# Kernel optimization log

Measured on AMD Instinct MI355X. Metric: run time of the kernel, lower is better.

## Reference

```python
import jax, jax.numpy as jnp
import numpy as np

IN_FEATURES = 512
OUT_FEATURES = 128
KERNEL_DIM = 32
BATCH = 128


def setup_inputs() -> dict:
    key = jax.random.key(0)
    kx, kT = jax.random.split(key)
    x = jax.random.normal(kx, (BATCH, IN_FEATURES), dtype=jnp.float32)
    # nn.Parameter initialized with normal(0, 1)
    T = jax.random.normal(kT, (IN_FEATURES, OUT_FEATURES, KERNEL_DIM), dtype=jnp.float32)
    return {"x": x, "T": T}


def reference(x, T):
    B = x.shape[0]
    in_f, out_f, k_dim = T.shape
    # projection: [B, in] @ [in, out*k] -> [B, out, k]
    m = (x @ T.reshape(in_f, out_f * k_dim)).reshape(B, out_f, k_dim)
    # pairwise L1 distance over kernel dim: [B, B, out]
    # original: M = m[None], M_T = m[:, None]; norm = |M - M_T|.sum(3); o_b = exp(-norm).sum(0) - 1
    norm = jnp.abs(m[None, :, :, :] - m[:, None, :, :]).sum(axis=-1)  # [i=B, j=B, out]
    o_b = jnp.exp(-norm).sum(axis=0) - 1.0  # [B, out] (subtract self-distance term exp(0)=1)
    return jnp.concatenate([x, o_b], axis=1)  # [B, in + out]
```

## Files before the change

### kernel.cpp

```cpp
#include <hip/hip_runtime.h>

#define B_SZ    128
#define IN_F    512
#define OUT_F   128
#define NC      4096
#define KD      32
#define OUT_COLS 640
#define MO_PITCH 36
#define AS_PITCH 136
#define BK      128

typedef __attribute__((ext_vector_type(8))) short  bf16x8;
typedef __attribute__((ext_vector_type(4))) float  f32x4;

static __device__ __forceinline__ unsigned short f2bfu(float f) {
    return (unsigned short)(__float_as_uint(f) >> 16);
}

__global__ __launch_bounds__(256) void prep_kernel(
    const float* __restrict__ x, float* __restrict__ out,
    unsigned short* __restrict__ xb)
{
    int idx = blockIdx.x * 256 + threadIdx.x;
    int b = idx >> 7, c4 = idx & 127;
    float4 v = ((const float4*)x)[idx];
    *(float4*)(out + b * OUT_COLS + c4 * 4) = v;
    ushort4 w;
    w.x = f2bfu(v.x); w.y = f2bfu(v.y); w.z = f2bfu(v.z); w.w = f2bfu(v.w);
    *(ushort4*)(xb + idx * 4) = w;
}

__global__ __launch_bounds__(512, 2) void gemm_kernel(
    const unsigned short* __restrict__ xb,
    const float* __restrict__ T,
    float* __restrict__ m)
{
    __shared__ unsigned short as[64 * AS_PITCH];
    __shared__ unsigned short bs[32 * AS_PITCH];

    const int tid  = threadIdx.x;
    const int lane = tid & 63;
    const int w    = tid >> 6;
    const int col  = lane & 15;
    const int q    = lane >> 4;
    const int n0   = blockIdx.x * 32;
    const int m0   = blockIdx.y * 64;
    const int mt   = w >> 1, nt = w & 1;

    f32x4 acc = {0.f, 0.f, 0.f, 0.f};

    for (int k0 = 0; k0 < IN_F; k0 += BK) {
        __syncthreads();
        #pragma unroll
        for (int p = 0; p < 2; ++p) {
            int u = tid + p * 512;
            int row = u >> 4, o8 = u & 15;
            uint4 v = *(const uint4*)(xb + (m0 + row) * IN_F + k0 + o8 * 8);
            *(uint4*)&as[row * AS_PITCH + o8 * 8] = v;
        }
        #pragma unroll
        for (int p = 0; p < 2; ++p) {
            int u = tid + p * 512;
            int kk = u >> 3, nq = u & 7;
            float4 v = *(const float4*)(T + (size_t)(k0 + kk) * NC + n0 + nq * 4);
            int nb = nq * 4;
            bs[(nb + 0) * AS_PITCH + kk] = f2bfu(v.x);
            bs[(nb + 1) * AS_PITCH + kk] = f2bfu(v.y);
            bs[(nb + 2) * AS_PITCH + kk] = f2bfu(v.z);
            bs[(nb + 3) * AS_PITCH + kk] = f2bfu(v.w);
        }
        __syncthreads();
        #pragma unroll
        for (int kt = 0; kt < 4; ++kt) {
            const int krel = kt * 32 + q * 8;
            bf16x8 af = *(const bf16x8*)&as[(mt * 16 + col) * AS_PITCH + krel];
            bf16x8 bf = *(const bf16x8*)&bs[(nt * 16 + col) * AS_PITCH + krel];
            acc = __builtin_amdgcn_mfma_f32_16x16x32_bf16(af, bf, acc, 0, 0, 0);
        }
    }
    float* dst = m + (size_t)(m0 + mt * 16 + q * 4) * NC + n0 + nt * 16 + col;
    dst[0 * NC] = acc[0]; dst[1 * NC] = acc[1];
    dst[2 * NC] = acc[2]; dst[3 * NC] = acc[3];
}

__global__ __launch_bounds__(1024, 4) void pairwise_kernel(
    const float* __restrict__ m,
    float* __restrict__ out)
{
    __shared__ float mo[B_SZ * MO_PITCH];
    __shared__ float psum[64 * 16];

    const int tid   = threadIdx.x;
    const int o     = blockIdx.x >> 1;
    const int jhalf = blockIdx.x & 1;

    {
        const int b = tid >> 3, k4 = tid & 7;
        float4 v = *(const float4*)(m + (size_t)b * NC + o * KD + k4 * 4);
        *(float4*)&mo[b * MO_PITCH + k4 * 4] = v;
    }
    __syncthreads();

    const int jj  = tid & 63;
    const int isl = tid >> 6;
    const int j   = jhalf * 64 + jj;

    float mj[KD];
    #pragma unroll
    for (int k4 = 0; k4 < 8; ++k4) {
        float4 v = *(const float4*)&mo[j * MO_PITCH + k4 * 4];
        mj[k4*4+0] = v.x; mj[k4*4+1] = v.y; mj[k4*4+2] = v.z; mj[k4*4+3] = v.w;
    }

    float s = 0.f;
    const int i0 = isl * 8;
    for (int i = i0; i < i0 + 8; ++i) {
        float norm = 0.f;
        #pragma unroll
        for (int k4 = 0; k4 < 8; ++k4) {
            float4 v = *(const float4*)&mo[i * MO_PITCH + k4 * 4];
            norm += fabsf(mj[k4*4+0] - v.x) + fabsf(mj[k4*4+1] - v.y)
                  + fabsf(mj[k4*4+2] - v.z) + fabsf(mj[k4*4+3] - v.w);
        }
        s += __expf(-norm);
    }
    psum[jj * 16 + isl] = s;
    __syncthreads();
    if (tid < 64) {
        float tot = 0.f;
        #pragma unroll
        for (int u = 0; u < 16; ++u) tot += psum[tid * 16 + u];
        out[(jhalf * 64 + tid) * OUT_COLS + IN_F + o] = tot - 1.0f;
    }
}

extern "C" void kernel_launch(void* const* d_in, const int* in_sizes, int n_in,
                              void* d_out, int out_size, void* d_ws, size_t ws_size,
                              hipStream_t stream) {
    const float* x = (const float*)d_in[0];
    const float* T = (const float*)d_in[1];
    float* out = (float*)d_out;
    float* m = (float*)d_ws;
    unsigned short* xb = (unsigned short*)((char*)d_ws + (2u << 20));

    prep_kernel<<<64, 256, 0, stream>>>(x, out, xb);
    gemm_kernel<<<dim3(128, 2), 512, 0, stream>>>(xb, T, m);
    pairwise_kernel<<<256, 1024, 0, stream>>>(m, out);
}
```

Baseline: 72.87 us.

## Fuse prep, GEMM and pairwise L1 kernels into a single kernel

```diff
diff --git a/kernel.cpp b/kernel.cpp
--- a/kernel.cpp
+++ b/kernel.cpp
@@ -1,13 +1,10 @@
 #include <hip/hip_runtime.h>
 
-#define B_SZ    128
 #define IN_F    512
-#define OUT_F   128
 #define NC      4096
-#define KD      32
 #define OUT_COLS 640
+#define AS_PITCH 136
 #define MO_PITCH 36
-#define AS_PITCH 136
 #define BK      128
 
 typedef __attribute__((ext_vector_type(8))) short  bf16x8;
@@ -16,54 +13,54 @@
 static __device__ __forceinline__ unsigned short f2bfu(float f) {
     return (unsigned short)(__float_as_uint(f) >> 16);
 }
-
-__global__ __launch_bounds__(256) void prep_kernel(
-    const float* __restrict__ x, float* __restrict__ out,
-    unsigned short* __restrict__ xb)
-{
-    int idx = blockIdx.x * 256 + threadIdx.x;
-    int b = idx >> 7, c4 = idx & 127;
-    float4 v = ((const float4*)x)[idx];
-    *(float4*)(out + b * OUT_COLS + c4 * 4) = v;
-    ushort4 w;
-    w.x = f2bfu(v.x); w.y = f2bfu(v.y); w.z = f2bfu(v.z); w.w = f2bfu(v.w);
-    *(ushort4*)(xb + idx * 4) = w;
+static __device__ __forceinline__ unsigned int pack2(float lo, float hi) {
+    return (__float_as_uint(lo) >> 16) | (__float_as_uint(hi) & 0xFFFF0000u);
 }
 
-__global__ __launch_bounds__(512, 2) void gemm_kernel(
-    const unsigned short* __restrict__ xb,
+__global__ __launch_bounds__(1024, 4) void fused_kernel(
+    const float* __restrict__ x,
     const float* __restrict__ T,
-    float* __restrict__ m)
+    float* __restrict__ out)
 {
-    __shared__ unsigned short as[64 * AS_PITCH];
-    __shared__ unsigned short bs[32 * AS_PITCH];
+    __shared__ __align__(16) char smem[51968];
+    unsigned short* as = (unsigned short*)smem;
+    unsigned short* bs = (unsigned short*)(smem + 34816);
+    float* mo   = (float*)smem;
+    float* psum = (float*)(smem + 43520);
 
-    const int tid  = threadIdx.x;
-    const int lane = tid & 63;
-    const int w    = tid >> 6;
-    const int col  = lane & 15;
-    const int q    = lane >> 4;
-    const int n0   = blockIdx.x * 32;
-    const int m0   = blockIdx.y * 64;
-    const int mt   = w >> 1, nt = w & 1;
+    const int tid   = threadIdx.x;
+    const int lane  = tid & 63;
+    const int w     = tid >> 6;
+    const int col   = lane & 15;
+    const int q     = lane >> 4;
+    const int o     = blockIdx.x >> 1;
+    const int jhalf = blockIdx.x & 1;
+    const int mt    = w >> 1;
+    const int nt    = w & 1;
+
+    if (tid < 64) {
+        int idx = blockIdx.x * 64 + tid;
+        int b = idx >> 7, c4 = idx & 127;
+        float4 v = ((const float4*)x)[idx];
+        *(float4*)(out + b * OUT_COLS + c4 * 4) = v;
+    }
 
     f32x4 acc = {0.f, 0.f, 0.f, 0.f};
-
     for (int k0 = 0; k0 < IN_F; k0 += BK) {
         __syncthreads();
         #pragma unroll
-        for (int p = 0; p < 2; ++p) {
-            int u = tid + p * 512;
-            int row = u >> 4, o8 = u & 15;
-            uint4 v = *(const uint4*)(xb + (m0 + row) * IN_F + k0 + o8 * 8);
-            *(uint4*)&as[row * AS_PITCH + o8 * 8] = v;
+        for (int p = 0; p < 4; ++p) {
+            int u   = tid + p * 1024;
+            int row = u >> 5, c4 = u & 31;
+            float4 v = *(const float4*)(x + row * IN_F + k0 + c4 * 4);
+            uint2 pv;
+            pv.x = pack2(v.x, v.y); pv.y = pack2(v.z, v.w);
+            *(uint2*)(as + row * AS_PITCH + c4 * 4) = pv;
         }
-        #pragma unroll
-        for (int p = 0; p < 2; ++p) {
-            int u = tid + p * 512;
-            int kk = u >> 3, nq = u & 7;
-            float4 v = *(const float4*)(T + (size_t)(k0 + kk) * NC + n0 + nq * 4);
-            int nb = nq * 4;
+        {
+            int kk = tid >> 3, cq = tid & 7;
+            float4 v = *(const float4*)(T + (size_t)(k0 + kk) * NC + o * 32 + cq * 4);
+            int nb = cq * 4;
             bs[(nb + 0) * AS_PITCH + kk] = f2bfu(v.x);
             bs[(nb + 1) * AS_PITCH + kk] = f2bfu(v.y);
             bs[(nb + 2) * AS_PITCH + kk] = f2bfu(v.z);
@@ -73,64 +70,57 @@
         #pragma unroll
         for (int kt = 0; kt < 4; ++kt) {
             const int krel = kt * 32 + q * 8;
-            bf16x8 af = *(const bf16x8*)&as[(mt * 16 + col) * AS_PITCH + krel];
-            bf16x8 bf = *(const bf16x8*)&bs[(nt * 16 + col) * AS_PITCH + krel];
-            acc = __builtin_amdgcn_mfma_f32_16x16x32_bf16(af, bf, acc, 0, 0, 0);
+            bf16x8 af  = *(const bf16x8*)(as + (mt * 16 + col) * AS_PITCH + krel);
+            bf16x8 bfr = *(const bf16x8*)(bs + (nt * 16 + col) * AS_PITCH + krel);
+            acc = __builtin_amdgcn_mfma_f32_16x16x32_bf16(af, bfr, acc, 0, 0, 0);
         }
     }
-    float* dst = m + (size_t)(m0 + mt * 16 + q * 4) * NC + n0 + nt * 16 + col;
-    dst[0 * NC] = acc[0]; dst[1 * NC] = acc[1];
-    dst[2 * NC] = acc[2]; dst[3 * NC] = acc[3];
-}
-
-__global__ __launch_bounds__(1024, 4) void pairwise_kernel(
-    const float* __restrict__ m,
-    float* __restrict__ out)
-{
-    __shared__ float mo[B_SZ * MO_PITCH];
-    __shared__ float psum[64 * 16];
-
-    const int tid   = threadIdx.x;
-    const int o     = blockIdx.x >> 1;
-    const int jhalf = blockIdx.x & 1;
-
+    __syncthreads();
     {
-        const int b = tid >> 3, k4 = tid & 7;
-        float4 v = *(const float4*)(m + (size_t)b * NC + o * KD + k4 * 4);
-        *(float4*)&mo[b * MO_PITCH + k4 * 4] = v;
+        float* dst = mo + (size_t)(mt * 16 + q * 4) * MO_PITCH + nt * 16 + col;
+        dst[0 * MO_PITCH] = acc[0]; dst[1 * MO_PITCH] = acc[1];
+        dst[2 * MO_PITCH] = acc[2]; dst[3 * MO_PITCH] = acc[3];
     }
     __syncthreads();
 
-    const int jj  = tid & 63;
-    const int isl = tid >> 6;
-    const int j   = jhalf * 64 + jj;
+    const int jj5 = tid & 31;
+    const int isl = tid >> 5;
+    const int j0  = jhalf * 64 + jj5;
 
-    float mj[KD];
+    float mj0[32], mj1[32];
     #pragma unroll
     for (int k4 = 0; k4 < 8; ++k4) {
-        float4 v = *(const float4*)&mo[j * MO_PITCH + k4 * 4];
-        mj[k4*4+0] = v.x; mj[k4*4+1] = v.y; mj[k4*4+2] = v.z; mj[k4*4+3] = v.w;
+        float4 a = *(const float4*)(mo + (size_t)j0 * MO_PITCH + k4 * 4);
+        float4 b = *(const float4*)(mo + (size_t)(j0 + 32) * MO_PITCH + k4 * 4);
+        mj0[k4*4+0] = a.x; mj0[k4*4+1] = a.y; mj0[k4*4+2] = a.z; mj0[k4*4+3] = a.w;
+        mj1[k4*4+0] = b.x; mj1[k4*4+1] = b.y; mj1[k4*4+2] = b.z; mj1[k4*4+3] = b.w;
     }
 
-    float s = 0.f;
-    const int i0 = isl * 8;
-    for (int i = i0; i < i0 + 8; ++i) {
-        float norm = 0.f;
+    float s0 = 0.f, s1 = 0.f;
+    #pragma unroll
+    for (int ii = 0; ii < 4; ++ii) {
+        const int i = isl * 4 + ii;
+        float n0 = 0.f, n1 = 0.f;
         #pragma unroll
         for (int k4 = 0; k4 < 8; ++k4) {
-            float4 v = *(const float4*)&mo[i * MO_PITCH + k4 * 4];
-            norm += fabsf(mj[k4*4+0] - v.x) + fabsf(mj[k4*4+1] - v.y)
-                  + fabsf(mj[k4*4+2] - v.z) + fabsf(mj[k4*4+3] - v.w);
+            float4 v = *(const float4*)(mo + (size_t)i * MO_PITCH + k4 * 4);
+            n0 += fabsf(mj0[k4*4+0] - v.x) + fabsf(mj0[k4*4+1] - v.y)
+                + fabsf(mj0[k4*4+2] - v.z) + fabsf(mj0[k4*4+3] - v.w);
+            n1 += fabsf(mj1[k4*4+0] - v.x) + fabsf(mj1[k4*4+1] - v.y)
+                + fabsf(mj1[k4*4+2] - v.z) + fabsf(mj1[k4*4+3] - v.w);
         }
-        s += __expf(-norm);
+        s0 += __expf(-n0);
+        s1 += __expf(-n1);
     }
-    psum[jj * 16 + isl] = s;
+    psum[jj5 * 33 + isl]        = s0;
+    psum[1056 + jj5 * 33 + isl] = s1;
     __syncthreads();
     if (tid < 64) {
+        int jsel = tid >> 5, jj = tid & 31;
         float tot = 0.f;
         #pragma unroll
-        for (int u = 0; u < 16; ++u) tot += psum[tid * 16 + u];
-        out[(jhalf * 64 + tid) * OUT_COLS + IN_F + o] = tot - 1.0f;
+        for (int u = 0; u < 32; ++u) tot += psum[jsel * 1056 + jj * 33 + u];
+        out[(jhalf * 64 + jsel * 32 + jj) * OUT_COLS + IN_F + o] = tot - 1.0f;
     }
 }
 
@@ -140,10 +130,7 @@
     const float* x = (const float*)d_in[0];
     const float* T = (const float*)d_in[1];
     float* out = (float*)d_out;
-    float* m = (float*)d_ws;
-    unsigned short* xb = (unsigned short*)((char*)d_ws + (2u << 20));
+    (void)d_ws; (void)ws_size;
 
-    prep_kernel<<<64, 256, 0, stream>>>(x, out, xb);
-    gemm_kernel<<<dim3(128, 2), 512, 0, stream>>>(xb, T, m);
-    pairwise_kernel<<<256, 1024, 0, stream>>>(m, out);
+    fused_kernel<<<256, 1024, 0, stream>>>(x, T, out);
 }
```

New measurement: 75.98 us. +4.3%, slower.
